# Kernel optimization log

Hardware: AMD Instinct MI355X
Metric: run time of the kernel (lower is better)

## Reference

```python
import jax, jax.numpy as jnp
import numpy as np

N_NODES = 50000
N_EDGES = 800000


def _sage(x, src, dst, Wl, bl, Wr):
    # mean-aggregate neighbor features (messages flow src -> dst), then linear
    msg = x[src]                                              # [E, d_in]
    s = jax.ops.segment_sum(msg, dst, num_segments=N_NODES)   # [N, d_in]
    cnt = jax.ops.segment_sum(jnp.ones((src.shape[0],), x.dtype), dst,
                              num_segments=N_NODES)           # [N]
    agg = s / jnp.maximum(cnt, 1.0)[:, None]
    return agg @ Wl.T + bl + x @ Wr.T


def setup_inputs() -> dict:
    key = jax.random.key(0)
    ks = jax.random.split(key, 10)
    d_in, h = 128, 64
    def w(k, o, i):
        return jax.random.normal(k, (o, i), jnp.float32) * (1.0 / np.sqrt(i))
    return {
        "x": jax.random.normal(ks[0], (N_NODES, d_in), jnp.float32),
        "edge_index": jax.random.randint(ks[1], (2, N_EDGES), 0, N_NODES, jnp.int64),
        "Wl1": w(ks[2], h, d_in), "bl1": jnp.zeros((h,), jnp.float32), "Wr1": w(ks[3], h, d_in),
        "Wl2": w(ks[4], 2 * h, h), "bl2": jnp.zeros((2 * h,), jnp.float32), "Wr2": w(ks[5], 2 * h, h),
        "Wl3": w(ks[6], 2 * h, 2 * h), "bl3": jnp.zeros((2 * h,), jnp.float32), "Wr3": w(ks[7], 2 * h, 2 * h),
        "Wl4": w(ks[8], h, 2 * h), "bl4": jnp.zeros((h,), jnp.float32), "Wr4": w(ks[9], h, 2 * h),
    }


def reference(x, edge_index, Wl1, bl1, Wr1, Wl2, bl2, Wr2, Wl3, bl3, Wr3, Wl4, bl4, Wr4):
    src, dst = edge_index[0], edge_index[1]
    h = jax.nn.relu(_sage(x, src, dst, Wl1, bl1, Wr1))
    h = jax.nn.relu(_sage(h, src, dst, Wl2, bl2, Wr2))
    h = jax.nn.relu(_sage(h, src, dst, Wl3, bl3, Wr3))
    h = _sage(h, src, dst, Wl4, bl4, Wr4)
    return h
```

## Files before the change

### kernel.cpp

```cpp
#include <hip/hip_runtime.h>

#define NN 50000
#define NE 800000
#define GB 391
#define NBUK 196
#define PB 128
#define CH 6250
#define HLEN (NBUK * PB)
#define SAB (HLEN / 256)

typedef __attribute__((ext_vector_type(8))) short short8v;
typedef __attribute__((ext_vector_type(4))) float float4v;
typedef __attribute__((ext_vector_type(2))) float float2v;
typedef __attribute__((ext_vector_type(2))) unsigned short ushort2v;

__device__ __forceinline__ int uni(int v) { return __builtin_amdgcn_readfirstlane(v); }
__device__ __forceinline__ unsigned short f2bf(float f) {
    unsigned u = __float_as_uint(f);
    return (unsigned short)((u + 0x7FFFu + ((u >> 16) & 1u)) >> 16);
}
__device__ __forceinline__ float bf2f(unsigned short h) {
    return __uint_as_float(((unsigned)h) << 16);
}

__global__ __launch_bounds__(256) void hist_kernel(const int* __restrict__ dst,
                                                   int* __restrict__ H) {
    __shared__ int h[NBUK];
    const int t = threadIdx.x;
    const int b = blockIdx.x;
    if (t < NBUK) h[t] = 0;
    __syncthreads();
    const int e0 = b * CH;
    for (int i = t; i < CH; i += 256) {
        int e = e0 + i;
        if (e < NE) atomicAdd(&h[dst[e] >> 8], 1);
    }
    __syncthreads();
    if (t < NBUK) H[t * PB + b] = h[t];
}

__global__ __launch_bounds__(256) void scanA_kernel(const int* __restrict__ a,
                                                    int* __restrict__ part) {
    __shared__ int red[256];
    const int t = threadIdx.x;
    red[t] = a[blockIdx.x * 256 + t];
    __syncthreads();
#pragma unroll
    for (int d = 128; d > 0; d >>= 1) {
        if (t < d) red[t] += red[t + d];
        __syncthreads();
    }
    if (t == 0) part[blockIdx.x] = red[0];
}

__global__ __launch_bounds__(128) void scanB_kernel(int* __restrict__ part) {
    __shared__ int ps[128];
    const int t = threadIdx.x;
    ps[t] = (t < SAB) ? part[t] : 0;
    __syncthreads();
#pragma unroll
    for (int d = 1; d < 128; d <<= 1) {
        int v = (t >= d) ? ps[t - d] : 0;
        __syncthreads();
        ps[t] += v;
        __syncthreads();
    }
    if (t < SAB) part[t] = (t == 0) ? 0 : ps[t - 1];
}

__global__ __launch_bounds__(256) void scanC_kernel(int* __restrict__ a,
                                                    const int* __restrict__ part) {
    __shared__ int ps[256];
    const int t = threadIdx.x;
    const int i = blockIdx.x * 256 + t;
    const int c = a[i];
    ps[t] = c;
    __syncthreads();
#pragma unroll
    for (int d = 1; d < 256; d <<= 1) {
        int v = (t >= d) ? ps[t - d] : 0;
        __syncthreads();
        ps[t] += v;
        __syncthreads();
    }
    a[i] = part[blockIdx.x] + ps[t] - c;
}

__global__ __launch_bounds__(256) void partition_kernel(const int* __restrict__ src,
                                                        const int* __restrict__ dst,
                                                        const int* __restrict__ Hs,
                                                        unsigned* __restrict__ tmp) {
    __shared__ int cur[NBUK];
    const int t = threadIdx.x;
    const int b = blockIdx.x;
    if (t < NBUK) cur[t] = Hs[t * PB + b];
    __syncthreads();
    const int e0 = b * CH;
    for (int i = t; i < CH; i += 256) {
        int e = e0 + i;
        if (e < NE) {
            const int d = dst[e];
            const int k = d >> 8;
            const int pos = atomicAdd(&cur[k], 1);
            tmp[pos] = (unsigned)src[e] | ((unsigned)(d & 255) << 16);
        }
    }
}

__global__ __launch_bounds__(256) void finalize_kernel(const unsigned* __restrict__ tmp,
                                                       const int* __restrict__ Hs,
                                                       int* __restrict__ off,
                                                       int* __restrict__ cnt,
                                                       float* __restrict__ inv,
                                                       unsigned short* __restrict__ srcs) {
    __shared__ int hist[256];
    __shared__ int ps[256];
    __shared__ int cur[256];
    const int t = threadIdx.x;
    const int k = blockIdx.x;
    const int s0 = Hs[k * PB];
    const int end = (k == NBUK - 1) ? NE : Hs[(k + 1) * PB];
    const int m = end - s0;
    hist[t] = 0;
    __syncthreads();
    for (int i = t; i < m; i += 256) {
        atomicAdd(&hist[(tmp[s0 + i] >> 16) & 255], 1);
    }
    __syncthreads();
    const int c = hist[t];
    ps[t] = c;
    __syncthreads();
#pragma unroll
    for (int d = 1; d < 256; d <<= 1) {
        int v = (t >= d) ? ps[t - d] : 0;
        __syncthreads();
        ps[t] += v;
        __syncthreads();
    }
    const int ex = ps[t] - c;
    const int node = k * 256 + t;
    if (node < NN) {
        off[node] = s0 + ex;
        cnt[node] = c;
        inv[node] = 1.0f / (float)max(c, 1);
    }
    cur[t] = s0 + ex;
    __syncthreads();
    for (int i = t; i < m; i += 256) {
        const unsigned u = tmp[s0 + i];
        const int p = atomicAdd(&cur[(u >> 16) & 255], 1);
        srcs[p] = (unsigned short)(u & 0xFFFFu);
    }
}

template<int D, int MODE, int DUALB>
__global__ __launch_bounds__(256) void gather_kernel(
    const unsigned short* __restrict__ yb, int ys, const unsigned short* __restrict__ srcs,
    const int* __restrict__ off, const int* __restrict__ cnt,
    const float* __restrict__ inv, const float* __restrict__ pre, int ps,
    float* __restrict__ out, int os, unsigned short* __restrict__ outb) {
    const int w = (blockIdx.x * blockDim.x + threadIdx.x) >> 6;
    const int lane = threadIdx.x & 63;
    if (w >= NN) return;
    const int o = uni(off[w]);
    const int n = uni(cnt[w]);
    const int h = lane >> 5;
    const int l = lane & 31;

    float a0 = 0.0f, a1 = 0.0f, a2 = 0.0f, a3 = 0.0f;
    int i = 0;
    for (; i + 8 <= n; i += 8) {
        int e0 = __builtin_nontemporal_load(&srcs[o + i + h]);
        int e1 = __builtin_nontemporal_load(&srcs[o + i + 2 + h]);
        int e2 = __builtin_nontemporal_load(&srcs[o + i + 4 + h]);
        int e3 = __builtin_nontemporal_load(&srcs[o + i + 6 + h]);
        if constexpr (D == 64) {
            const ushort2 v0 = *reinterpret_cast<const ushort2*>(&yb[(size_t)e0 * ys + 2 * l]);
            const ushort2 v1 = *reinterpret_cast<const ushort2*>(&yb[(size_t)e1 * ys + 2 * l]);
            const ushort2 v2 = *reinterpret_cast<const ushort2*>(&yb[(size_t)e2 * ys + 2 * l]);
            const ushort2 v3 = *reinterpret_cast<const ushort2*>(&yb[(size_t)e3 * ys + 2 * l]);
            a0 += bf2f(v0.x) + bf2f(v1.x) + bf2f(v2.x) + bf2f(v3.x);
            a1 += bf2f(v0.y) + bf2f(v1.y) + bf2f(v2.y) + bf2f(v3.y);
        } else {
            const ushort4 v0 = *reinterpret_cast<const ushort4*>(&yb[(size_t)e0 * ys + 4 * l]);
            const ushort4 v1 = *reinterpret_cast<const ushort4*>(&yb[(size_t)e1 * ys + 4 * l]);
            const ushort4 v2 = *reinterpret_cast<const ushort4*>(&yb[(size_t)e2 * ys + 4 * l]);
            const ushort4 v3 = *reinterpret_cast<const ushort4*>(&yb[(size_t)e3 * ys + 4 * l]);
            a0 += bf2f(v0.x) + bf2f(v1.x) + bf2f(v2.x) + bf2f(v3.x);
            a1 += bf2f(v0.y) + bf2f(v1.y) + bf2f(v2.y) + bf2f(v3.y);
            a2 += bf2f(v0.z) + bf2f(v1.z) + bf2f(v2.z) + bf2f(v3.z);
            a3 += bf2f(v0.w) + bf2f(v1.w) + bf2f(v2.w) + bf2f(v3.w);
        }
    }
    for (; i + 2 <= n; i += 2) {
        int e = __builtin_nontemporal_load(&srcs[o + i + h]);
        if constexpr (D == 64) {
            const ushort2 v = *reinterpret_cast<const ushort2*>(&yb[(size_t)e * ys + 2 * l]);
            a0 += bf2f(v.x);
            a1 += bf2f(v.y);
        } else {
            const ushort4 v = *reinterpret_cast<const ushort4*>(&yb[(size_t)e * ys + 4 * l]);
            a0 += bf2f(v.x); a1 += bf2f(v.y); a2 += bf2f(v.z); a3 += bf2f(v.w);
        }
    }
    if (i < n && h == 0) {
        int e = __builtin_nontemporal_load(&srcs[o + i]);
        if constexpr (D == 64) {
            const ushort2 v = *reinterpret_cast<const ushort2*>(&yb[(size_t)e * ys + 2 * l]);
            a0 += bf2f(v.x);
            a1 += bf2f(v.y);
        } else {
            const ushort4 v = *reinterpret_cast<const ushort4*>(&yb[(size_t)e * ys + 4 * l]);
            a0 += bf2f(v.x); a1 += bf2f(v.y); a2 += bf2f(v.z); a3 += bf2f(v.w);
        }
    }
    a0 += __shfl_xor(a0, 32, 64);
    a1 += __shfl_xor(a1, 32, 64);
    if constexpr (D == 128) {
        a2 += __shfl_xor(a2, 32, 64);
        a3 += __shfl_xor(a3, 32, 64);
    }
    if (h != 0) return;

    const float iv = inv[w];
    if constexpr (D == 64) {
        float r0 = a0 * iv, r1 = a1 * iv;
        if constexpr (MODE != 0) {
            const float2v pv = __builtin_nontemporal_load(
                reinterpret_cast<const float2v*>(&pre[(size_t)w * ps + 2 * l]));
            r0 += pv.x; r1 += pv.y;
        }
        if constexpr (MODE == 1) { r0 = fmaxf(r0, 0.0f); r1 = fmaxf(r1, 0.0f); }
        float2v sv = {r0, r1};
        __builtin_nontemporal_store(sv, reinterpret_cast<float2v*>(&out[(size_t)w * os + 2 * l]));
        if constexpr (DUALB) {
            ushort2v bv = {f2bf(r0), f2bf(r1)};
            __builtin_nontemporal_store(bv, reinterpret_cast<ushort2v*>(&outb[(size_t)w * 64 + 2 * l]));
        }
    } else {
        float r0 = a0 * iv, r1 = a1 * iv, r2 = a2 * iv, r3 = a3 * iv;
        if constexpr (MODE != 0) {
            const float4v pv = __builtin_nontemporal_load(
                reinterpret_cast<const float4v*>(&pre[(size_t)w * ps + 4 * l]));
            r0 += pv.x; r1 += pv.y; r2 += pv.z; r3 += pv.w;
        }
        if constexpr (MODE == 1) {
            r0 = fmaxf(r0, 0.0f); r1 = fmaxf(r1, 0.0f);
            r2 = fmaxf(r2, 0.0f); r3 = fmaxf(r3, 0.0f);
        }
        float4v sv = {r0, r1, r2, r3};
        __builtin_nontemporal_store(sv, reinterpret_cast<float4v*>(&out[(size_t)w * os + 4 * l]));
    }
}

struct WSrc { const float* p[8]; };

__global__ __launch_bounds__(256) void wplanes_kernel(WSrc S,
                                                      unsigned short* __restrict__ ph,
                                                      unsigned short* __restrict__ pl) {
    const int e = blockIdx.x * 256 + threadIdx.x;
    const int seg = blockIdx.y;
    const int row = e >> 7, k = e & 127;
    float x;
    switch (seg) {
        case 0:  x = (row < 64) ? S.p[0][row * 128 + k] : S.p[1][(row - 64) * 128 + k]; break;
        case 1:  x = (k < 64)   ? S.p[2][row * 64 + k]  : S.p[3][row * 64 + (k - 64)];  break;
        case 2:  x = S.p[4][e]; break;
        case 3:  x = S.p[5][e]; break;
        default: x = (row < 64) ? S.p[6][row * 128 + k] : S.p[7][(row - 64) * 128 + k]; break;
    }
    const unsigned u = __float_as_uint(x);
    const float lo = x - __uint_as_float(u & 0xFFFF0000u);
    const int o = seg * 16384 + e;
    ph[o] = (unsigned short)(u >> 16);
    pl[o] = (unsigned short)(__float_as_uint(lo) >> 16);
}

struct GemmArgs {
    const unsigned short* Bh; const unsigned short* Bl;
    float* out0; const float* bias0; int os0, obf0;
    float* out1; const float* bias1; int os1, obf1;
    int relu;
};

__global__ __launch_bounds__(256) void gemm_mfma(const float* __restrict__ in,
                                                 GemmArgs A0, GemmArgs A1) {
    const GemmArgs G = blockIdx.y ? A1 : A0;
    const int t = threadIdx.x;
    const int lane = t & 63;
    const int wid = t >> 6;
    const int wn = wid & 1;
    const int wc = wid >> 1;
    const int l15 = lane & 15;
    const int lk = lane >> 4;
    const int nb = (int)blockIdx.x * 128 + wn * 64;

    float* const outp = wc ? G.out1 : G.out0;
    const float* const biasp = wc ? G.bias1 : G.bias0;
    const int os = wc ? G.os1 : G.os0;
    const int obf = wc ? G.obf1 : G.obf0;
    const unsigned short* const Bhp = G.Bh + (size_t)(wc * 64) * 128;
    const unsigned short* const Blp = G.Bl + (size_t)(wc * 64) * 128;
    const ptrdiff_t dlo = Blp - Bhp;

    float4v acc[4][4];
#pragma unroll
    for (int mi = 0; mi < 4; ++mi)
#pragma unroll
        for (int ci = 0; ci < 4; ++ci) acc[mi][ci] = (float4v)0.0f;

    const float* arow[4];
#pragma unroll
    for (int mi = 0; mi < 4; ++mi) {
        int r = nb + mi * 16 + l15;
        if (r > NN - 1) r = NN - 1;
        arow[mi] = in + (size_t)r * 128;
    }
    const unsigned short* brow[4];
#pragma unroll
    for (int ci = 0; ci < 4; ++ci) brow[ci] = Bhp + (size_t)(ci * 16 + l15) * 128;

    for (int ks = 0; ks < 4; ++ks) {
        const int ko = ks * 32 + lk * 8;
        short8v Ah[4], Al[4];
#pragma unroll
        for (int mi = 0; mi < 4; ++mi) {
            const float4v v0 = __builtin_nontemporal_load(
                reinterpret_cast<const float4v*>(arow[mi] + ko));
            const float4v v1 = __builtin_nontemporal_load(
                reinterpret_cast<const float4v*>(arow[mi] + ko + 4));
            float xv[8] = {v0.x, v0.y, v0.z, v0.w, v1.x, v1.y, v1.z, v1.w};
            union { unsigned u[4]; short8v s; } H, L;
#pragma unroll
            for (int q = 0; q < 4; ++q) {
                const unsigned u0 = __float_as_uint(xv[2 * q]);
                const unsigned u1 = __float_as_uint(xv[2 * q + 1]);
                const float l0 = xv[2 * q]     - __uint_as_float(u0 & 0xFFFF0000u);
                const float l1 = xv[2 * q + 1] - __uint_as_float(u1 & 0xFFFF0000u);
                H.u[q] = (u1 & 0xFFFF0000u) | (u0 >> 16);
                L.u[q] = (__float_as_uint(l1) & 0xFFFF0000u) | (__float_as_uint(l0) >> 16);
            }
            Ah[mi] = H.s;
            Al[mi] = L.s;
        }
        short8v Bhf[4], Blf[4];
#pragma unroll
        for (int ci = 0; ci < 4; ++ci) {
            Bhf[ci] = *reinterpret_cast<const short8v*>(brow[ci] + ko);
            Blf[ci] = *reinterpret_cast<const short8v*>(brow[ci] + dlo + ko);
        }
#pragma unroll
        for (int mi = 0; mi < 4; ++mi)
#pragma unroll
            for (int ci = 0; ci < 4; ++ci) {
                acc[mi][ci] = __builtin_amdgcn_mfma_f32_16x16x32_bf16(Ah[mi], Bhf[ci], acc[mi][ci], 0, 0, 0);
                acc[mi][ci] = __builtin_amdgcn_mfma_f32_16x16x32_bf16(Ah[mi], Blf[ci], acc[mi][ci], 0, 0, 0);
                acc[mi][ci] = __builtin_amdgcn_mfma_f32_16x16x32_bf16(Al[mi], Bhf[ci], acc[mi][ci], 0, 0, 0);
            }
    }

#pragma unroll
    for (int ci = 0; ci < 4; ++ci) {
        const int c = ci * 16 + l15;
        const float b = biasp ? biasp[c] : 0.0f;
#pragma unroll
        for (int mi = 0; mi < 4; ++mi) {
#pragma unroll
            for (int j = 0; j < 4; ++j) {
                const int r = nb + mi * 16 + lk * 4 + j;
                if (r < NN) {
                    float v = acc[mi][ci][j] + b;
                    if (G.relu) v = fmaxf(v, 0.0f);
                    if (obf) {
                        __builtin_nontemporal_store(
                            f2bf(v), &((unsigned short*)outp)[(size_t)r * os + c]);
                    } else {
                        __builtin_nontemporal_store(v, &outp[(size_t)r * os + c]);
                    }
                }
            }
        }
    }
}

extern "C" void kernel_launch(void* const* d_in, const int* in_sizes, int n_in,
                              void* d_out, int out_size, void* d_ws, size_t ws_size,
                              hipStream_t stream) {
    const float* x   = (const float*)d_in[0];
    const int*   eix = (const int*)d_in[1];
    const float* Wl1 = (const float*)d_in[2];
    const float* bl1 = (const float*)d_in[3];
    const float* Wr1 = (const float*)d_in[4];
    const float* Wl2 = (const float*)d_in[5];
    const float* bl2 = (const float*)d_in[6];
    const float* Wr2 = (const float*)d_in[7];
    const float* Wl3 = (const float*)d_in[8];
    const float* bl3 = (const float*)d_in[9];
    const float* Wr3 = (const float*)d_in[10];
    const float* Wl4 = (const float*)d_in[11];
    const float* bl4 = (const float*)d_in[12];
    const float* Wr4 = (const float*)d_in[13];
    float* out = (float*)d_out;

    const int* src = eix;
    const int* dst = eix + NE;

    char* ws = (char*)d_ws;
    int*   cnt  = (int*)ws;
    int*   off  = cnt + NN;
    float* inv  = (float*)(off + NN);
    int*   Hs   = (int*)(inv + NN);
    int*   part = Hs + HLEN;
    unsigned short* srcs = (unsigned short*)(part + 256);
    unsigned short* ph = srcs + NE;
    unsigned short* pl = ph + 81920;
    unsigned short* XB1 = pl + 81920;
    unsigned short* H1B = XB1 + (size_t)NN * 64;
    unsigned short* G3B = XB1;
    float* HCAT = (float*)(XB1 + (size_t)NN * 128);
    float* H2   = HCAT + (size_t)NN * 128;
    float* HPRE = H2 + (size_t)NN * 128;
    unsigned*       tmp = (unsigned*)HPRE;
    unsigned short* G4B = (unsigned short*)HCAT;

    hist_kernel<<<PB, 256, 0, stream>>>(dst, Hs);
    scanA_kernel<<<SAB, 256, 0, stream>>>(Hs, part);
    scanB_kernel<<<1, 128, 0, stream>>>(part);
    scanC_kernel<<<SAB, 256, 0, stream>>>(Hs, part);
    partition_kernel<<<PB, 256, 0, stream>>>(src, dst, Hs, tmp);
    finalize_kernel<<<NBUK, 256, 0, stream>>>(tmp, Hs, off, cnt, inv, srcs);

    {
        WSrc s;
        s.p[0] = Wl1; s.p[1] = Wr1; s.p[2] = Wl2; s.p[3] = Wr2;
        s.p[4] = Wl3; s.p[5] = Wr3; s.p[6] = Wl4; s.p[7] = Wr4;
        wplanes_kernel<<<dim3(64, 5), 256, 0, stream>>>(s, ph, pl);
    }

    {
        GemmArgs a{ph, pl, (float*)XB1, nullptr, 64, 1, HCAT + 64, bl1, 128, 0, 0};
        gemm_mfma<<<dim3(GB, 1), 256, 0, stream>>>(x, a, a);
    }
    gather_kernel<64, 1, 1><<<12500, 256, 0, stream>>>(
        XB1, 64, srcs, off, cnt, inv, HCAT + 64, 128, HCAT + 64, 128, H1B);

    gather_kernel<64, 0, 0><<<12500, 256, 0, stream>>>(
        H1B, 64, srcs, off, cnt, inv, nullptr, 0, HCAT, 128, nullptr);
    {
        GemmArgs a{ph + 16384, pl + 16384, H2, bl2, 128, 0, H2 + 64, bl2 + 64, 128, 0, 1};
        gemm_mfma<<<dim3(GB, 1), 256, 0, stream>>>(HCAT, a, a);
    }

    {
        GemmArgs a0{ph + 2 * 16384, pl + 2 * 16384,
                    (float*)G3B, nullptr, 128, 1,
                    (float*)(G3B + 64), nullptr, 128, 1, 0};
        GemmArgs a1{ph + 3 * 16384, pl + 3 * 16384,
                    HPRE, bl3, 128, 0,
                    HPRE + 64, bl3 + 64, 128, 0, 0};
        gemm_mfma<<<dim3(GB, 2), 256, 0, stream>>>(H2, a0, a1);
    }
    gather_kernel<128, 1, 0><<<12500, 256, 0, stream>>>(
        G3B, 128, srcs, off, cnt, inv, HPRE, 128, HPRE, 128, nullptr);

    {
        GemmArgs a{ph + 4 * 16384, pl + 4 * 16384,
                   (float*)G4B, nullptr, 64, 1, out, bl4, 64, 0, 0};
        gemm_mfma<<<dim3(GB, 1), 256, 0, stream>>>(HPRE, a, a);
    }
    gather_kernel<64, 2, 0><<<12500, 256, 0, stream>>>(
        G4B, 64, srcs, off, cnt, inv, out, 64, out, 64, nullptr);
}
```

Baseline: 395.6 us.

## Store intermediate activations as bf16 hi/lo planes instead of fp32

Gather and GEMM kernels now write intermediate activations as pre-split bf16 high and low planes. Downstream GEMMs load those planes directly and no longer reload fp32 and split it per tile, which cuts A-side conversion ALU work and keeps the bytes moved equal. The layer-3 dual-grid GEMM is split into two launches, nontemporal hints are removed throughout, and the workspace is re-laid out. The hi/lo split keeps roughly fp32 accuracy, at the cost of an extra launch and extra split work in the producer epilogues.

```diff
diff --git a/kernel.cpp b/kernel.cpp
--- a/kernel.cpp
+++ b/kernel.cpp
@@ -11,8 +11,6 @@
 
 typedef __attribute__((ext_vector_type(8))) short short8v;
 typedef __attribute__((ext_vector_type(4))) float float4v;
-typedef __attribute__((ext_vector_type(2))) float float2v;
-typedef __attribute__((ext_vector_type(2))) unsigned short ushort2v;
 
 __device__ __forceinline__ int uni(int v) { return __builtin_amdgcn_readfirstlane(v); }
 __device__ __forceinline__ unsigned short f2bf(float f) {
@@ -153,12 +151,13 @@
     }
 }
 
-template<int D, int MODE, int DUALB>
+template<int D, int MODE, int PLANES>
 __global__ __launch_bounds__(256) void gather_kernel(
     const unsigned short* __restrict__ yb, int ys, const unsigned short* __restrict__ srcs,
     const int* __restrict__ off, const int* __restrict__ cnt,
     const float* __restrict__ inv, const float* __restrict__ pre, int ps,
-    float* __restrict__ out, int os, unsigned short* __restrict__ outb) {
+    float* __restrict__ out, int os,
+    unsigned short* __restrict__ outh, unsigned short* __restrict__ outl, int os2) {
     const int w = (blockIdx.x * blockDim.x + threadIdx.x) >> 6;
     const int lane = threadIdx.x & 63;
     if (w >= NN) return;
@@ -170,10 +169,10 @@
     float a0 = 0.0f, a1 = 0.0f, a2 = 0.0f, a3 = 0.0f;
     int i = 0;
     for (; i + 8 <= n; i += 8) {
-        int e0 = __builtin_nontemporal_load(&srcs[o + i + h]);
-        int e1 = __builtin_nontemporal_load(&srcs[o + i + 2 + h]);
-        int e2 = __builtin_nontemporal_load(&srcs[o + i + 4 + h]);
-        int e3 = __builtin_nontemporal_load(&srcs[o + i + 6 + h]);
+        int e0 = srcs[o + i + h];
+        int e1 = srcs[o + i + 2 + h];
+        int e2 = srcs[o + i + 4 + h];
+        int e3 = srcs[o + i + 6 + h];
         if constexpr (D == 64) {
             const ushort2 v0 = *reinterpret_cast<const ushort2*>(&yb[(size_t)e0 * ys + 2 * l]);
             const ushort2 v1 = *reinterpret_cast<const ushort2*>(&yb[(size_t)e1 * ys + 2 * l]);
@@ -193,7 +192,7 @@
         }
     }
     for (; i + 2 <= n; i += 2) {
-        int e = __builtin_nontemporal_load(&srcs[o + i + h]);
+        int e = srcs[o + i + h];
         if constexpr (D == 64) {
             const ushort2 v = *reinterpret_cast<const ushort2*>(&yb[(size_t)e * ys + 2 * l]);
             a0 += bf2f(v.x);
@@ -204,7 +203,7 @@
         }
     }
     if (i < n && h == 0) {
-        int e = __builtin_nontemporal_load(&srcs[o + i]);
+        int e = srcs[o + i];
         if constexpr (D == 64) {
             const ushort2 v = *reinterpret_cast<const ushort2*>(&yb[(size_t)e * ys + 2 * l]);
             a0 += bf2f(v.x);
@@ -226,30 +225,41 @@
     if constexpr (D == 64) {
         float r0 = a0 * iv, r1 = a1 * iv;
         if constexpr (MODE != 0) {
-            const float2v pv = __builtin_nontemporal_load(
-                reinterpret_cast<const float2v*>(&pre[(size_t)w * ps + 2 * l]));
+            const float2 pv = *reinterpret_cast<const float2*>(&pre[(size_t)w * ps + 2 * l]);
             r0 += pv.x; r1 += pv.y;
         }
         if constexpr (MODE == 1) { r0 = fmaxf(r0, 0.0f); r1 = fmaxf(r1, 0.0f); }
-        float2v sv = {r0, r1};
-        __builtin_nontemporal_store(sv, reinterpret_cast<float2v*>(&out[(size_t)w * os + 2 * l]));
-        if constexpr (DUALB) {
-            ushort2v bv = {f2bf(r0), f2bf(r1)};
-            __builtin_nontemporal_store(bv, reinterpret_cast<ushort2v*>(&outb[(size_t)w * 64 + 2 * l]));
+        if constexpr (PLANES) {
+            const unsigned short h0 = f2bf(r0), h1v = f2bf(r1);
+            ushort2 hv = {h0, h1v};
+            ushort2 lv = {f2bf(r0 - bf2f(h0)), f2bf(r1 - bf2f(h1v))};
+            *reinterpret_cast<ushort2*>(&outh[(size_t)w * os2 + 2 * l]) = hv;
+            *reinterpret_cast<ushort2*>(&outl[(size_t)w * os2 + 2 * l]) = lv;
+        } else {
+            float2 sv = {r0, r1};
+            *reinterpret_cast<float2*>(&out[(size_t)w * os + 2 * l]) = sv;
         }
     } else {
         float r0 = a0 * iv, r1 = a1 * iv, r2 = a2 * iv, r3 = a3 * iv;
         if constexpr (MODE != 0) {
-            const float4v pv = __builtin_nontemporal_load(
-                reinterpret_cast<const float4v*>(&pre[(size_t)w * ps + 4 * l]));
+            const float4 pv = *reinterpret_cast<const float4*>(&pre[(size_t)w * ps + 4 * l]);
             r0 += pv.x; r1 += pv.y; r2 += pv.z; r3 += pv.w;
         }
         if constexpr (MODE == 1) {
             r0 = fmaxf(r0, 0.0f); r1 = fmaxf(r1, 0.0f);
             r2 = fmaxf(r2, 0.0f); r3 = fmaxf(r3, 0.0f);
         }
-        float4v sv = {r0, r1, r2, r3};
-        __builtin_nontemporal_store(sv, reinterpret_cast<float4v*>(&out[(size_t)w * os + 4 * l]));
+        if constexpr (PLANES) {
+            const unsigned short h0 = f2bf(r0), h1v = f2bf(r1), h2 = f2bf(r2), h3 = f2bf(r3);
+            ushort4 hv = {h0, h1v, h2, h3};
+            ushort4 lv = {f2bf(r0 - bf2f(h0)), f2bf(r1 - bf2f(h1v)),
+                          f2bf(r2 - bf2f(h2)), f2bf(r3 - bf2f(h3))};
+            *reinterpret_cast<ushort4*>(&outh[(size_t)w * os2 + 4 * l]) = hv;
+            *reinterpret_cast<ushort4*>(&outl[(size_t)w * os2 + 4 * l]) = lv;
+        } else {
+            float4 sv = {r0, r1, r2, r3};
+            *reinterpret_cast<float4*>(&out[(size_t)w * os + 4 * l]) = sv;
+        }
     }
 }
 
@@ -278,14 +288,16 @@
 
 struct GemmArgs {
     const unsigned short* Bh; const unsigned short* Bl;
-    float* out0; const float* bias0; int os0, obf0;
-    float* out1; const float* bias1; int os1, obf1;
+    float* out0; unsigned short* outl0; const float* bias0; int os0, om0;
+    float* out1; unsigned short* outl1; const float* bias1; int os1, om1;
     int relu;
 };
 
-__global__ __launch_bounds__(256) void gemm_mfma(const float* __restrict__ in,
-                                                 GemmArgs A0, GemmArgs A1) {
-    const GemmArgs G = blockIdx.y ? A1 : A0;
+template<int APLANES>
+__global__ __launch_bounds__(256) void gemm_mfma(
+    const float* __restrict__ inf,
+    const unsigned short* __restrict__ inh, const unsigned short* __restrict__ inl,
+    GemmArgs G) {
     const int t = threadIdx.x;
     const int lane = t & 63;
     const int wid = t >> 6;
@@ -296,9 +308,10 @@
     const int nb = (int)blockIdx.x * 128 + wn * 64;
 
     float* const outp = wc ? G.out1 : G.out0;
+    unsigned short* const outlp = wc ? G.outl1 : G.outl0;
     const float* const biasp = wc ? G.bias1 : G.bias0;
     const int os = wc ? G.os1 : G.os0;
-    const int obf = wc ? G.obf1 : G.obf0;
+    const int om = wc ? G.om1 : G.om0;
     const unsigned short* const Bhp = G.Bh + (size_t)(wc * 64) * 128;
     const unsigned short* const Blp = G.Bl + (size_t)(wc * 64) * 128;
     const ptrdiff_t dlo = Blp - Bhp;
@@ -309,12 +322,11 @@
 #pragma unroll
         for (int ci = 0; ci < 4; ++ci) acc[mi][ci] = (float4v)0.0f;
 
-    const float* arow[4];
+    int arowi[4];
 #pragma unroll
     for (int mi = 0; mi < 4; ++mi) {
         int r = nb + mi * 16 + l15;
-        if (r > NN - 1) r = NN - 1;
-        arow[mi] = in + (size_t)r * 128;
+        arowi[mi] = (r > NN - 1) ? NN - 1 : r;
     }
     const unsigned short* brow[4];
 #pragma unroll
@@ -325,23 +337,28 @@
         short8v Ah[4], Al[4];
 #pragma unroll
         for (int mi = 0; mi < 4; ++mi) {
-            const float4v v0 = __builtin_nontemporal_load(
-                reinterpret_cast<const float4v*>(arow[mi] + ko));
-            const float4v v1 = __builtin_nontemporal_load(
-                reinterpret_cast<const float4v*>(arow[mi] + ko + 4));
-            float xv[8] = {v0.x, v0.y, v0.z, v0.w, v1.x, v1.y, v1.z, v1.w};
-            union { unsigned u[4]; short8v s; } H, L;
-#pragma unroll
-            for (int q = 0; q < 4; ++q) {
-                const unsigned u0 = __float_as_uint(xv[2 * q]);
-                const unsigned u1 = __float_as_uint(xv[2 * q + 1]);
-                const float l0 = xv[2 * q]     - __uint_as_float(u0 & 0xFFFF0000u);
-                const float l1 = xv[2 * q + 1] - __uint_as_float(u1 & 0xFFFF0000u);
-                H.u[q] = (u1 & 0xFFFF0000u) | (u0 >> 16);
-                L.u[q] = (__float_as_uint(l1) & 0xFFFF0000u) | (__float_as_uint(l0) >> 16);
+            if constexpr (APLANES) {
+                const size_t b = (size_t)arowi[mi] * 128 + ko;
+                Ah[mi] = *reinterpret_cast<const short8v*>(inh + b);
+                Al[mi] = *reinterpret_cast<const short8v*>(inl + b);
+            } else {
+                const float* ar = inf + (size_t)arowi[mi] * 128;
+                const float4v v0 = *reinterpret_cast<const float4v*>(ar + ko);
+                const float4v v1 = *reinterpret_cast<const float4v*>(ar + ko + 4);
+                float xv[8] = {v0.x, v0.y, v0.z, v0.w, v1.x, v1.y, v1.z, v1.w};
+                union { unsigned u[4]; short8v s; } H, L;
+#pragma unroll
+                for (int q = 0; q < 4; ++q) {
+                    const unsigned u0 = __float_as_uint(xv[2 * q]);
+                    const unsigned u1 = __float_as_uint(xv[2 * q + 1]);
+                    const float l0 = xv[2 * q]     - __uint_as_float(u0 & 0xFFFF0000u);
+                    const float l1 = xv[2 * q + 1] - __uint_as_float(u1 & 0xFFFF0000u);
+                    H.u[q] = (u1 & 0xFFFF0000u) | (u0 >> 16);
+                    L.u[q] = (__float_as_uint(l1) & 0xFFFF0000u) | (__float_as_uint(l0) >> 16);
+                }
+                Ah[mi] = H.s;
+                Al[mi] = L.s;
             }
-            Ah[mi] = H.s;
-            Al[mi] = L.s;
         }
         short8v Bhf[4], Blf[4];
 #pragma unroll
@@ -371,11 +388,14 @@
                 if (r < NN) {
                     float v = acc[mi][ci][j] + b;
                     if (G.relu) v = fmaxf(v, 0.0f);
-                    if (obf) {
-                        __builtin_nontemporal_store(
-                            f2bf(v), &((unsigned short*)outp)[(size_t)r * os + c]);
+                    if (om == 0) {
+                        outp[(size_t)r * os + c] = v;
+                    } else if (om == 1) {
+                        ((unsigned short*)outp)[(size_t)r * os + c] = f2bf(v);
                     } else {
-                        __builtin_nontemporal_store(v, &outp[(size_t)r * os + c]);
+                        const unsigned short hv = f2bf(v);
+                        ((unsigned short*)outp)[(size_t)r * os + c] = hv;
+                        outlp[(size_t)r * os + c] = f2bf(v - bf2f(hv));
                     }
                 }
             }
@@ -414,14 +434,23 @@
     unsigned short* srcs = (unsigned short*)(part + 256);
     unsigned short* ph = srcs + NE;
     unsigned short* pl = ph + 81920;
-    unsigned short* XB1 = pl + 81920;
-    unsigned short* H1B = XB1 + (size_t)NN * 64;
-    unsigned short* G3B = XB1;
-    float* HCAT = (float*)(XB1 + (size_t)NN * 128);
-    float* H2   = HCAT + (size_t)NN * 128;
-    float* HPRE = H2 + (size_t)NN * 128;
-    unsigned*       tmp = (unsigned*)HPRE;
-    unsigned short* G4B = (unsigned short*)HCAT;
+    char* R1 = (char*)(pl + 81920);
+    char* R2 = R1 + (size_t)NN * 128 * 4;
+    char* R3 = R2 + (size_t)NN * 128 * 4;
+    char* R4 = R3 + (size_t)NN * 128 * 2;
+
+    unsigned short* XB1 = (unsigned short*)R1;
+    float*          P1  = (float*)(R1 + (size_t)NN * 64 * 2);
+    unsigned short* H2h = (unsigned short*)R1;
+    unsigned short* H2l = H2h + (size_t)NN * 128;
+    unsigned short* HCh = (unsigned short*)R2;
+    unsigned short* HCl = HCh + (size_t)NN * 128;
+    unsigned short* H3h = HCh;
+    unsigned short* H3l = HCl;
+    unsigned short* G3B = (unsigned short*)R3;
+    unsigned short* G4B = (unsigned short*)R3;
+    unsigned* tmp  = (unsigned*)R4;
+    float*    HPRE = (float*)R4;
 
     hist_kernel<<<PB, 256, 0, stream>>>(dst, Hs);
     scanA_kernel<<<SAB, 256, 0, stream>>>(Hs, part);
@@ -438,36 +467,44 @@
     }
 
     {
-        GemmArgs a{ph, pl, (float*)XB1, nullptr, 64, 1, HCAT + 64, bl1, 128, 0, 0};
-        gemm_mfma<<<dim3(GB, 1), 256, 0, stream>>>(x, a, a);
+        GemmArgs a{ph, pl,
+                   (float*)XB1, nullptr, nullptr, 64, 1,
+                   P1, nullptr, bl1, 64, 0, 0};
+        gemm_mfma<0><<<GB, 256, 0, stream>>>(x, nullptr, nullptr, a);
     }
     gather_kernel<64, 1, 1><<<12500, 256, 0, stream>>>(
-        XB1, 64, srcs, off, cnt, inv, HCAT + 64, 128, HCAT + 64, 128, H1B);
-
-    gather_kernel<64, 0, 0><<<12500, 256, 0, stream>>>(
-        H1B, 64, srcs, off, cnt, inv, nullptr, 0, HCAT, 128, nullptr);
+        XB1, 64, srcs, off, cnt, inv, P1, 64, nullptr, 0, HCh + 64, HCl + 64, 128);
+
+    gather_kernel<64, 0, 1><<<12500, 256, 0, stream>>>(
+        HCh + 64, 128, srcs, off, cnt, inv, nullptr, 0, nullptr, 0, HCh, HCl, 128);
     {
-        GemmArgs a{ph + 16384, pl + 16384, H2, bl2, 128, 0, H2 + 64, bl2 + 64, 128, 0, 1};
-        gemm_mfma<<<dim3(GB, 1), 256, 0, stream>>>(HCAT, a, a);
+        GemmArgs a{ph + 16384, pl + 16384,
+                   (float*)H2h, H2l, bl2, 128, 2,
+                   (float*)(H2h + 64), H2l + 64, bl2 + 64, 128, 2, 1};
+        gemm_mfma<1><<<GB, 256, 0, stream>>>(nullptr, HCh, HCl, a);
     }
 
     {
-        GemmArgs a0{ph + 2 * 16384, pl + 2 * 16384,
-                    (float*)G3B, nullptr, 128, 1,
-                    (float*)(G3B + 64), nullptr, 128, 1, 0};
-        GemmArgs a1{ph + 3 * 16384, pl + 3 * 16384,
-                    HPRE, bl3, 128, 0,
-                    HPRE + 64, bl3 + 64, 128, 0, 0};
-        gemm_mfma<<<dim3(GB, 2), 256, 0, stream>>>(H2, a0, a1);
-    }
-    gather_kernel<128, 1, 0><<<12500, 256, 0, stream>>>(
-        G3B, 128, srcs, off, cnt, inv, HPRE, 128, HPRE, 128, nullptr);
+        GemmArgs a{ph + 2 * 16384, pl + 2 * 16384,
+                   (float*)G3B, nullptr, nullptr, 128, 1,
+                   (float*)(G3B + 64), nullptr, nullptr, 128, 1, 0};
+        gemm_mfma<1><<<GB, 256, 0, stream>>>(nullptr, H2h, H2l, a);
+    }
+    {
+        GemmArgs a{ph + 3 * 16384, pl + 3 * 16384,
+                   HPRE, nullptr, bl3, 128, 0,
+                   HPRE + 64, nullptr, bl3 + 64, 128, 0, 0};
+        gemm_mfma<1><<<GB, 256, 0, stream>>>(nullptr, H2h, H2l, a);
+    }
+    gather_kernel<128, 1, 1><<<12500, 256, 0, stream>>>(
+        G3B, 128, srcs, off, cnt, inv, HPRE, 128, nullptr, 0, H3h, H3l, 128);
 
     {
         GemmArgs a{ph + 4 * 16384, pl + 4 * 16384,
-                   (float*)G4B, nullptr, 64, 1, out, bl4, 64, 0, 0};
-        gemm_mfma<<<dim3(GB, 1), 256, 0, stream>>>(HPRE, a, a);
+                   (float*)G4B, nullptr, nullptr, 64, 1,
+                   out, nullptr, bl4, 64, 0, 0};
+        gemm_mfma<1><<<GB, 256, 0, stream>>>(nullptr, H3h, H3l, a);
     }
     gather_kernel<64, 2, 0><<<12500, 256, 0, stream>>>(
-        G4B, 64, srcs, off, cnt, inv, out, 64, out, 64, nullptr);
-}
+        G4B, 64, srcs, off, cnt, inv, out, 64, out, 64, nullptr, nullptr, 0);
+}
```

After: 346.9 us. 1.14x faster.
